# Performance work log

Measured on AMD Instinct MI355X. Metric: run time of the kernel, lower is better.

## Reference

```python
import jax, jax.numpy as jnp
import numpy as np

EPS = 1e-5

def _conv2d(x, w, b, pad):
    # NCHW conv, stride 1
    out = jax.lax.conv_general_dilated(x, w, (1, 1), [(pad, pad), (pad, pad)],
                                       dimension_numbers=('NCHW', 'OIHW', 'NCHW'))
    return out + b[None, :, None, None]

def _deform_conv2d(x, offset, mask, weight, bias, pad):
    # torchvision.ops.deform_conv2d (modulated, stride=1, dilation=1)
    B, C, H, W = x.shape
    O, _, K, _ = weight.shape
    kk = K * K
    off = offset.reshape(B, kk, 2, H, W)
    dy, dx = off[:, :, 0], off[:, :, 1]          # [B,kk,H,W]
    ki = (jnp.arange(kk) // K).astype(x.dtype)
    kj = (jnp.arange(kk) % K).astype(x.dtype)
    hh = jnp.arange(H, dtype=x.dtype)
    ww = jnp.arange(W, dtype=x.dtype)
    ys = dy + (hh[None, :, None] + ki[:, None, None] - pad)[None]  # [B,kk,H,W]
    xs = dx + (ww[None, None, :] + kj[:, None, None] - pad)[None]
    y0 = jnp.floor(ys); x0 = jnp.floor(xs)
    wy = ys - y0; wx = xs - x0
    xf = x.reshape(B, C, H * W)

    def gather(yi, xi):
        valid = ((yi >= 0) & (yi <= H - 1) & (xi >= 0) & (xi <= W - 1)).astype(x.dtype)
        yc = jnp.clip(yi, 0, H - 1).astype(jnp.int32)
        xc = jnp.clip(xi, 0, W - 1).astype(jnp.int32)
        idx = (yc * W + xc).reshape(B, -1)
        v = jax.vmap(lambda f, i: f[:, i])(xf, idx).reshape(B, C, kk, H, W)
        return v * valid[:, None]

    one = jnp.asarray(1.0, x.dtype)
    sampled = (gather(y0, x0) * ((one - wy) * (one - wx))[:, None]
               + gather(y0, x0 + 1) * ((one - wy) * wx)[:, None]
               + gather(y0 + 1, x0) * (wy * (one - wx))[:, None]
               + gather(y0 + 1, x0 + 1) * (wy * wx)[:, None])
    sampled = sampled * mask[:, None]            # modulation
    out = jnp.einsum('bckhw,ock->bohw', sampled, weight.reshape(O, C, kk))
    return out + bias[None, :, None, None]

def setup_inputs() -> dict:
    key = jax.random.key(0)
    ks = jax.random.split(key, 7)
    B, C, H, W = 8, 768, 32, 32
    x = jax.random.normal(ks[0], (B, C, H, W), jnp.float32)
    proj_w = jax.random.normal(ks[1], (768, 768, 3, 3), jnp.float32) * 0.02
    proj_b = jax.random.normal(ks[2], (768,), jnp.float32) * 0.02
    offset_w = jax.random.normal(ks[3], (18, 768, 3, 3), jnp.float32) * 0.01
    offset_b = jax.random.normal(ks[4], (18,), jnp.float32) * 0.01
    mask_w = jax.random.normal(ks[5], (9, 768, 3, 3), jnp.float32) * 0.01
    mask_b = jax.random.normal(ks[6], (9,), jnp.float32) * 0.01
    gamma = jnp.ones((768,), jnp.float32)
    beta = jnp.zeros((768,), jnp.float32)
    return {"x": x, "proj_w": proj_w, "proj_b": proj_b, "offset_w": offset_w,
            "offset_b": offset_b, "mask_w": mask_w, "mask_b": mask_b,
            "gamma": gamma, "beta": beta}

def reference(x, proj_w, proj_b, offset_w, offset_b, mask_w, mask_b, gamma, beta):
    pad = 1
    H, W = x.shape[-2], x.shape[-1]
    max_off = float(min(H, W) // 4)
    offset = jnp.clip(_conv2d(x, offset_w, offset_b, pad), -max_off, max_off)
    mask = 2.0 * jax.nn.sigmoid(_conv2d(x, mask_w, mask_b, pad))
    y = _deform_conv2d(x, offset, mask, proj_w, proj_b, pad)
    # SyncBatchNorm (training-mode batch statistics, biased var)
    mean = jnp.mean(y, axis=(0, 2, 3))
    var = jnp.var(y, axis=(0, 2, 3))
    yn = (y - mean[None, :, None, None]) * jax.lax.rsqrt(var + EPS)[None, :, None, None]
    yn = yn * gamma[None, :, None, None] + beta[None, :, None, None]
    return x + jax.nn.gelu(yn, approximate=False)
```

## Files before the change

kernel.cpp:

```cpp
#include <hip/hip_runtime.h>
#include <math.h>

typedef __attribute__((ext_vector_type(4))) float f32x4;
typedef __attribute__((ext_vector_type(8))) short s16x8;
typedef __attribute__((ext_vector_type(4))) unsigned int u32x4;
typedef unsigned short ushort_t;

#define HW   1024
#define C_IN 768
#define B_N  8

__device__ inline ushort_t f2bf(float f) {
    unsigned u = __builtin_bit_cast(unsigned, f);
    unsigned r = u + 0x7FFFu + ((u >> 16) & 1u);
    return (ushort_t)(r >> 16);
}
__device__ inline float bf2f(short s) {
    return __builtin_bit_cast(float, ((unsigned)(ushort_t)s) << 16);
}

__global__ __launch_bounds__(256) void prepack_xt(
    const float* __restrict__ x, ushort_t* __restrict__ xt)
{
    __shared__ ushort_t tile[64][66];
    int bid = blockIdx.x;
    int b  = bid / 192;
    int r  = bid % 192;
    int cg = r / 16, pg = r % 16;
    int c0 = cg * 64, p0 = pg * 64;
    int t = threadIdx.x;
#pragma unroll
    for (int i = 0; i < 16; ++i) {
        int idx = t + i * 256;
        int cr = idx >> 6, col = idx & 63;
        tile[cr][col] = f2bf(x[(((size_t)b * C_IN + c0 + cr) << 10) + p0 + col]);
    }
    __syncthreads();
#pragma unroll
    for (int i = 0; i < 16; ++i) {
        int idx = t + i * 256;
        int pr = idx >> 6, col = idx & 63;
        xt[((size_t)(b << 10) + p0 + pr) * C_IN + c0 + col] = tile[col][pr];
    }
}

__global__ __launch_bounds__(256) void prepack_proj(
    const float* __restrict__ pw, ushort_t* __restrict__ A)
{
    int t = blockIdx.x * 256 + threadIdx.x;
    int lane = t & 63;
    int smi  = t >> 6;
    int s  = smi / 48, mf = smi - s * 48;
    int o  = mf * 16 + (lane & 15);
    int k0 = s * 32 + ((lane >> 4) << 3);
    int tap = k0 / 768;
    int c   = k0 - tap * 768;
    const float* src = pw + (size_t)o * 6912 + (size_t)c * 9 + tap;
    s16x8 pk;
#pragma unroll
    for (int e = 0; e < 8; ++e) pk[e] = (short)f2bf(src[e * 9]);
    *(s16x8*)(A + (size_t)smi * 512 + lane * 8) = pk;
}

__global__ __launch_bounds__(256) void prepack_om(
    const float* __restrict__ offw, const float* __restrict__ mskw,
    ushort_t* __restrict__ A2)
{
    int t = blockIdx.x * 256 + threadIdx.x;
    int lane = t & 63;
    int smi  = t >> 6;
    int s  = smi >> 1, mf = smi & 1;
    int oc = mf * 16 + (lane & 15);
    int k0 = s * 32 + ((lane >> 4) << 3);
    int tap = k0 / 768;
    int c   = k0 - tap * 768;
    s16x8 pk;
#pragma unroll
    for (int e = 0; e < 8; ++e) pk[e] = 0;
    if (oc < 27) {
        const float* src = (oc < 18)
            ? offw + ((size_t)oc        * 768 + c) * 9 + tap
            : mskw + ((size_t)(oc - 18) * 768 + c) * 9 + tap;
#pragma unroll
        for (int e = 0; e < 8; ++e) pk[e] = (short)f2bf(src[e * 9]);
    }
    *(s16x8*)(A2 + (size_t)smi * 512 + lane * 8) = pk;
}

__global__ __launch_bounds__(256) void offmask_mfma(
    const ushort_t* __restrict__ xt, const ushort_t* __restrict__ A2,
    const float* __restrict__ offb, const float* __restrict__ mbias,
    float* __restrict__ offs, float* __restrict__ maskb)
{
    int bid = blockIdx.x;
    int b = bid >> 5, pt = bid & 31;
    int p0 = pt << 5;
    int t = threadIdx.x, lane = t & 63, wv = t >> 6;
    int mf = wv >> 1, nf = wv & 1;
    int q = lane >> 4;
    int px = p0 + nf * 16 + (lane & 15);
    int h = px >> 5, w = px & 31;
    const char* xb = (const char*)xt + (size_t)b * (HW * 1536);
    f32x4 acc = (f32x4){0.f, 0.f, 0.f, 0.f};

    for (int tap = 0; tap < 9; ++tap) {
        int yy = h + tap / 3 - 1, xx = w + tap % 3 - 1;
        bool ok = (yy >= 0 && yy < 32 && xx >= 0 && xx < 32);
        int pos = ok ? (yy * 32 + xx) : 0;
        const char* bp = xb + (size_t)pos * 1536 + q * 16;
        for (int cs = 0; cs < 24; ++cs) {
            int s = tap * 24 + cs;
            s16x8 bf;
            if (ok) bf = *(const s16x8*)(bp + cs * 64);
            else    bf = (s16x8){0, 0, 0, 0, 0, 0, 0, 0};
            s16x8 af = *(const s16x8*)(A2 + ((size_t)(s * 2 + mf) * 64 + lane) * 8);
            acc = __builtin_amdgcn_mfma_f32_16x16x32_bf16(af, bf, acc, 0, 0, 0);
        }
    }
#pragma unroll
    for (int r = 0; r < 4; ++r) {
        int oc = mf * 16 + ((lane >> 4) << 2) + r;
        if (oc < 18) {
            float v = acc[r] + offb[oc];
            v = fminf(fmaxf(v, -8.f), 8.f);
            offs[((b * 18 + oc) << 10) + px] = v;
        } else if (oc < 27) {
            float v = acc[r] + mbias[oc - 18];
            maskb[((b * 9 + oc - 18) << 10) + px] = 2.f / (1.f + expf(-v));
        }
    }
}

__global__ __launch_bounds__(512, 4) void deform_mfma(
    const ushort_t* __restrict__ xt, const ushort_t* __restrict__ Amat,
    const float* __restrict__ offs, const float* __restrict__ maskb,
    float* __restrict__ y)
{
    __shared__ float4 meta_w[576];
    __shared__ int4   meta_i[576];
    __shared__ __align__(16) ushort_t Bs[2][64][64];

    int id = blockIdx.x;
    int b = id & 7;
    int pxt = (id >> 3) & 15;
    int otile = id >> 7;
    int p0 = pxt << 6;
    int t = threadIdx.x, lane = t & 63, wv = t >> 6;
    int wm = wv >> 1, wn = wv & 1;
    int q4 = lane >> 4;

    int bpx = wv * 8 + (lane >> 3);
    int oct = lane & 7;
    const int wchunk = (oct ^ (bpx & 7)) * 8;

    for (int i = t; i < 576; i += 512) {
        int k = i >> 6, j = i & 63;
        int hw = p0 + j, h = hw >> 5, w = hw & 31;
        float dy = offs[((b * 18 + 2 * k) << 10) + hw];
        float dx = offs[((b * 18 + 2 * k + 1) << 10) + hw];
        float m  = maskb[((b * 9 + k) << 10) + hw];
        float ys = dy + (float)(h + k / 3 - 1);
        float xs = dx + (float)(w + k % 3 - 1);
        float fy = floorf(ys), fx = floorf(xs);
        float wy = ys - fy, wx = xs - fx;
        int iy0 = (int)fy, ix0 = (int)fx;
        int iy1 = iy0 + 1, ix1 = ix0 + 1;
        float vy0 = (iy0 >= 0 && iy0 < 32) ? 1.f : 0.f;
        float vy1 = (iy1 >= 0 && iy1 < 32) ? 1.f : 0.f;
        float vx0 = (ix0 >= 0 && ix0 < 32) ? 1.f : 0.f;
        float vx1 = (ix1 >= 0 && ix1 < 32) ? 1.f : 0.f;
        int cy0 = min(max(iy0, 0), 31), cx0 = min(max(ix0, 0), 31);
        int cy1 = min(max(iy1, 0), 31), cx1 = min(max(ix1, 0), 31);
        float4 wv4;
        wv4.x = (1.f - wy) * (1.f - wx) * m * vy0 * vx0;
        wv4.y = (1.f - wy) * wx         * m * vy0 * vx1;
        wv4.z = wy         * (1.f - wx) * m * vy1 * vx0;
        wv4.w = wy         * wx         * m * vy1 * vx1;
        meta_w[i] = wv4;
        meta_i[i] = make_int4((cy0 * 32 + cx0) * 1536, (cy0 * 32 + cx1) * 1536,
                              (cy1 * 32 + cx0) * 1536, (cy1 * 32 + cx1) * 1536);
    }
    asm volatile("s_waitcnt lgkmcnt(0)" ::: "memory");
    __builtin_amdgcn_s_barrier();

    f32x4 acc[3][2];
#pragma unroll
    for (int f = 0; f < 3; ++f)
#pragma unroll
        for (int n = 0; n < 2; ++n) acc[f][n] = (f32x4){0.f, 0.f, 0.f, 0.f};

    const char* xb = (const char*)xt + (size_t)b * (HW * 1536);
    const int afrag0 = otile * 12 + wm * 3;

    s16x8 ga0, ga1, ga2, ga3, gb0, gb1, gb2, gb3;
    float4 w4a, w4b;

#define WBAR() do { asm volatile("s_waitcnt lgkmcnt(0)" ::: "memory"); \
                    __builtin_amdgcn_s_barrier(); } while (0)

#define ISSUE(G0, G1, G2, G3, W4, qq) do {                                  \
    int nt_ = (qq) / 12, nc_ = (qq) - nt_ * 12;                             \
    W4 = meta_w[nt_ * 64 + bpx];                                            \
    int4 i4_ = meta_i[nt_ * 64 + bpx];                                      \
    const char* bsrc_ = xb + nc_ * 128 + oct * 16;                          \
    G0 = *(const s16x8*)(bsrc_ + i4_.x);                                    \
    G1 = *(const s16x8*)(bsrc_ + i4_.y);                                    \
    G2 = *(const s16x8*)(bsrc_ + i4_.z);                                    \
    G3 = *(const s16x8*)(bsrc_ + i4_.w);                                    \
} while (0)

#define BUILD(G0, G1, G2, G3, W4, BUF) do {                                 \
    u32x4 bw_;                                                              \
    _Pragma("unroll")                                                       \
    for (int e2 = 0; e2 < 4; ++e2) {                                        \
        float v0_ = W4.x * bf2f(G0[2*e2])   + W4.y * bf2f(G1[2*e2])         \
                  + W4.z * bf2f(G2[2*e2])   + W4.w * bf2f(G3[2*e2]);        \
        float v1_ = W4.x * bf2f(G0[2*e2+1]) + W4.y * bf2f(G1[2*e2+1])       \
                  + W4.z * bf2f(G2[2*e2+1]) + W4.w * bf2f(G3[2*e2+1]);      \
        unsigned rr_;                                                       \
        asm("v_cvt_pk_bf16_f32 %0, %1, %2" : "=v"(rr_) : "v"(v0_), "v"(v1_)); \
        bw_[e2] = rr_;                                                      \
    }                                                                       \
    *(u32x4*)&Bs[BUF][bpx][wchunk] = bw_;                                   \
} while (0)

#define MFMA_PHASE(P, BUF) do {                                             \
    _Pragma("unroll")                                                       \
    for (int kk = 0; kk < 2; ++kk) {                                        \
        int s_ = 2 * (P) + kk;                                              \
        const s16x8* ap_ = (const s16x8*)(Amat +                            \
            ((size_t)(s_ * 48 + afrag0) * 64 + lane) * 8);                  \
        s16x8 a0_ = ap_[0], a1_ = ap_[64], a2_ = ap_[128];                  \
        int rc_ = ((kk * 4 + q4) ^ (lane & 7)) * 8;                         \
        s16x8 b0_ = *(const s16x8*)&Bs[BUF][wn * 32 + (lane & 15)][rc_];    \
        s16x8 b1_ = *(const s16x8*)&Bs[BUF][wn * 32 + 16 + (lane & 15)][rc_]; \
        acc[0][0] = __builtin_amdgcn_mfma_f32_16x16x32_bf16(a0_, b0_, acc[0][0], 0, 0, 0); \
        acc[0][1] = __builtin_amdgcn_mfma_f32_16x16x32_bf16(a0_, b1_, acc[0][1], 0, 0, 0); \
        acc[1][0] = __builtin_amdgcn_mfma_f32_16x16x32_bf16(a1_, b0_, acc[1][0], 0, 0, 0); \
        acc[1][1] = __builtin_amdgcn_mfma_f32_16x16x32_bf16(a1_, b1_, acc[1][1], 0, 0, 0); \
        acc[2][0] = __builtin_amdgcn_mfma_f32_16x16x32_bf16(a2_, b0_, acc[2][0], 0, 0, 0); \
        acc[2][1] = __builtin_amdgcn_mfma_f32_16x16x32_bf16(a2_, b1_, acc[2][1], 0, 0, 0); \
    }                                                                       \
} while (0)

    ISSUE(ga0, ga1, ga2, ga3, w4a, 0);
    ISSUE(gb0, gb1, gb2, gb3, w4b, 1);
    BUILD(ga0, ga1, ga2, ga3, w4a, 0);
    WBAR();

    for (int pp = 0; pp < 54; ++pp) {
        int pe = 2 * pp;
        if (pp < 53) ISSUE(ga0, ga1, ga2, ga3, w4a, pe + 2);
        MFMA_PHASE(pe, 0);
        BUILD(gb0, gb1, gb2, gb3, w4b, 1);
        WBAR();

        int po = pe + 1;
        if (pp < 53) ISSUE(gb0, gb1, gb2, gb3, w4b, po + 2);
        MFMA_PHASE(po, 1);
        if (pp < 53) BUILD(ga0, ga1, ga2, ga3, w4a, 0);
        WBAR();
    }

    int pxo = p0 + wn * 32 + (lane & 15);
    int obase = otile * 192 + wm * 48;
#pragma unroll
    for (int f = 0; f < 3; ++f) {
        int orow = obase + f * 16 + ((lane >> 4) << 2);
#pragma unroll
        for (int r = 0; r < 4; ++r) {
            size_t rowoff = ((size_t)(b * 768 + orow + r) << 10);
            y[rowoff + pxo]      = acc[f][0][r];
            y[rowoff + pxo + 16] = acc[f][1][r];
        }
    }
#undef WBAR
#undef ISSUE
#undef BUILD
#undef MFMA_PHASE
}

__global__ __launch_bounds__(256) void stats_kernel(
    const float* __restrict__ y, float* __restrict__ stats)
{
    int o = blockIdx.x;
    int tid = threadIdx.x;
    float s1 = 0.f, s2 = 0.f;
    for (int i = tid; i < B_N * HW; i += 256) {
        int b = i >> 10, hw = i & 1023;
        float v = y[(((size_t)b * 768 + o) << 10) + hw];
        s1 += v; s2 += v * v;
    }
#pragma unroll
    for (int off = 32; off > 0; off >>= 1) {
        s1 += __shfl_down(s1, off);
        s2 += __shfl_down(s2, off);
    }
    __shared__ float ls1[4], ls2[4];
    int wid = tid >> 6, lane = tid & 63;
    if (lane == 0) { ls1[wid] = s1; ls2[wid] = s2; }
    __syncthreads();
    if (tid == 0) {
        float t1 = ls1[0] + ls1[1] + ls1[2] + ls1[3];
        float t2 = ls2[0] + ls2[1] + ls2[2] + ls2[3];
        float mean = t1 * (1.0f / 8192.0f);
        float var  = t2 * (1.0f / 8192.0f) - mean * mean;
        stats[o]       = mean;
        stats[768 + o] = 1.0f / sqrtf(var + 1e-5f);
    }
}

__global__ __launch_bounds__(256) void finalize_kernel(
    const float* __restrict__ x, const float* __restrict__ stats,
    const float* __restrict__ gamma, const float* __restrict__ beta,
    float* __restrict__ y)
{
    const int total4 = B_N * 768 * HW / 4;
    for (int f = blockIdx.x * 256 + threadIdx.x; f < total4;
         f += gridDim.x * 256) {
        int e = f << 2;
        int o = (e >> 10) % 768;
        float mean = stats[o], rstd = stats[768 + o];
        float ga = gamma[o], be = beta[o];
        float4 v  = ((const float4*)y)[f];
        float4 xv = ((const float4*)x)[f];
        float4 r;
        {
            float yn = (v.x - mean) * rstd * ga + be;
            r.x = xv.x + 0.5f * yn * (1.0f + erff(yn * 0.70710678f));
        }
        {
            float yn = (v.y - mean) * rstd * ga + be;
            r.y = xv.y + 0.5f * yn * (1.0f + erff(yn * 0.70710678f));
        }
        {
            float yn = (v.z - mean) * rstd * ga + be;
            r.z = xv.z + 0.5f * yn * (1.0f + erff(yn * 0.70710678f));
        }
        {
            float yn = (v.w - mean) * rstd * ga + be;
            r.w = xv.w + 0.5f * yn * (1.0f + erff(yn * 0.70710678f));
        }
        ((float4*)y)[f] = r;
    }
}

extern "C" void kernel_launch(void* const* d_in, const int* in_sizes, int n_in,
                              void* d_out, int out_size, void* d_ws, size_t ws_size,
                              hipStream_t stream)
{
    const float* x        = (const float*)d_in[0];
    const float* proj_w   = (const float*)d_in[1];
    const float* offset_w = (const float*)d_in[3];
    const float* offset_b = (const float*)d_in[4];
    const float* mask_w   = (const float*)d_in[5];
    const float* mask_b   = (const float*)d_in[6];
    const float* gamma    = (const float*)d_in[7];
    const float* beta     = (const float*)d_in[8];

    char* ws = (char*)d_ws;
    float*    offs  = (float*)(ws);
    float*    maskb = (float*)(ws + 589824);
    float*    stats = (float*)(ws + 884736);
    ushort_t* A     = (ushort_t*)(ws + 890880);
    ushort_t* A2    = (ushort_t*)(ws + 11507712);
    ushort_t* xt    = (ushort_t*)(ws + 11950080);
    float* y = (float*)d_out;

    prepack_xt<<<1536, 256, 0, stream>>>(x, xt);
    prepack_om<<<108, 256, 0, stream>>>(offset_w, mask_w, A2);
    prepack_proj<<<2592, 256, 0, stream>>>(proj_w, A);
    offmask_mfma<<<256, 256, 0, stream>>>(xt, A2, offset_b, mask_b, offs, maskb);
    deform_mfma<<<512, 512, 0, stream>>>(xt, A, offs, maskb, y);
    stats_kernel<<<768, 256, 0, stream>>>(y, stats);
    finalize_kernel<<<2048, 256, 0, stream>>>(x, stats, gamma, beta, y);
}
```

Measured before the change: 270.6 us.

## Share each bilinear-sampled B tile across 384 output channels with 1024-thread blocks

The deformable-conv MFMA kernel now launches 256 blocks of 1024 threads instead of 512 blocks of 512, so each block covers 384 output channels instead of 192. Each sampled B tile is built once and consumed by 16 waves, which halves the redundant bilinear gather and interpolation work across output-channel tiles. Each thread now gathers and interpolates 4 bf16 values instead of 8. MFMA phases are also wrapped in s_setprio to favour matrix issue over the gather waves. The trade-off is fewer, larger blocks and potentially more barrier contention among 16 waves per block.

```diff
diff --git a/kernel.cpp b/kernel.cpp
--- a/kernel.cpp
+++ b/kernel.cpp
@@ -3,7 +3,7 @@
 
 typedef __attribute__((ext_vector_type(4))) float f32x4;
 typedef __attribute__((ext_vector_type(8))) short s16x8;
-typedef __attribute__((ext_vector_type(4))) unsigned int u32x4;
+typedef __attribute__((ext_vector_type(4))) short s16x4;
 typedef unsigned short ushort_t;
 
 #define HW   1024
@@ -131,7 +131,7 @@
     }
 }
 
-__global__ __launch_bounds__(512, 4) void deform_mfma(
+__global__ __launch_bounds__(1024, 4) void deform_mfma(
     const ushort_t* __restrict__ xt, const ushort_t* __restrict__ Amat,
     const float* __restrict__ offs, const float* __restrict__ maskb,
     float* __restrict__ y)
@@ -145,15 +145,16 @@
     int pxt = (id >> 3) & 15;
     int otile = id >> 7;
     int p0 = pxt << 6;
-    int t = threadIdx.x, lane = t & 63, wv = t >> 6;
-    int wm = wv >> 1, wn = wv & 1;
+    int t = threadIdx.x, lane = t & 63, wvid = t >> 6;
+    int wm = wvid >> 1, wn = wvid & 1;
     int q4 = lane >> 4;
 
-    int bpx = wv * 8 + (lane >> 3);
-    int oct = lane & 7;
-    const int wchunk = (oct ^ (bpx & 7)) * 8;
-
-    for (int i = t; i < 576; i += 512) {
+    int bpx  = t >> 4;
+    int sub  = t & 15;
+    int oct  = sub >> 1, half = sub & 1;
+    const int wchunk = (oct ^ (bpx & 7)) * 8 + half * 4;
+
+    for (int i = t; i < 576; i += 1024) {
         int k = i >> 6, j = i & 63;
         int hw = p0 + j, h = hw >> 5, w = hw & 31;
         float dy = offs[((b * 18 + 2 * k) << 10) + hw];
@@ -190,9 +191,9 @@
         for (int n = 0; n < 2; ++n) acc[f][n] = (f32x4){0.f, 0.f, 0.f, 0.f};
 
     const char* xb = (const char*)xt + (size_t)b * (HW * 1536);
-    const int afrag0 = otile * 12 + wm * 3;
-
-    s16x8 ga0, ga1, ga2, ga3, gb0, gb1, gb2, gb3;
+    const int afrag0 = otile * 24 + wm * 3;
+
+    s16x4 ga0, ga1, ga2, ga3, gb0, gb1, gb2, gb3;
     float4 w4a, w4b;
 
 #define WBAR() do { asm volatile("s_waitcnt lgkmcnt(0)" ::: "memory"); \
@@ -202,29 +203,36 @@
     int nt_ = (qq) / 12, nc_ = (qq) - nt_ * 12;                             \
     W4 = meta_w[nt_ * 64 + bpx];                                            \
     int4 i4_ = meta_i[nt_ * 64 + bpx];                                      \
-    const char* bsrc_ = xb + nc_ * 128 + oct * 16;                          \
-    G0 = *(const s16x8*)(bsrc_ + i4_.x);                                    \
-    G1 = *(const s16x8*)(bsrc_ + i4_.y);                                    \
-    G2 = *(const s16x8*)(bsrc_ + i4_.z);                                    \
-    G3 = *(const s16x8*)(bsrc_ + i4_.w);                                    \
+    const char* bsrc_ = xb + nc_ * 128 + sub * 8;                           \
+    G0 = *(const s16x4*)(bsrc_ + i4_.x);                                    \
+    G1 = *(const s16x4*)(bsrc_ + i4_.y);                                    \
+    G2 = *(const s16x4*)(bsrc_ + i4_.z);                                    \
+    G3 = *(const s16x4*)(bsrc_ + i4_.w);                                    \
 } while (0)
 
 #define BUILD(G0, G1, G2, G3, W4, BUF) do {                                 \
-    u32x4 bw_;                                                              \
-    _Pragma("unroll")                                                       \
-    for (int e2 = 0; e2 < 4; ++e2) {                                        \
-        float v0_ = W4.x * bf2f(G0[2*e2])   + W4.y * bf2f(G1[2*e2])         \
-                  + W4.z * bf2f(G2[2*e2])   + W4.w * bf2f(G3[2*e2]);        \
-        float v1_ = W4.x * bf2f(G0[2*e2+1]) + W4.y * bf2f(G1[2*e2+1])       \
-                  + W4.z * bf2f(G2[2*e2+1]) + W4.w * bf2f(G3[2*e2+1]);      \
-        unsigned rr_;                                                       \
-        asm("v_cvt_pk_bf16_f32 %0, %1, %2" : "=v"(rr_) : "v"(v0_), "v"(v1_)); \
-        bw_[e2] = rr_;                                                      \
+    uint2 bw_;                                                              \
+    unsigned r0_, r1_;                                                      \
+    {                                                                       \
+        float v0_ = W4.x * bf2f(G0[0]) + W4.y * bf2f(G1[0])                 \
+                  + W4.z * bf2f(G2[0]) + W4.w * bf2f(G3[0]);                \
+        float v1_ = W4.x * bf2f(G0[1]) + W4.y * bf2f(G1[1])                 \
+                  + W4.z * bf2f(G2[1]) + W4.w * bf2f(G3[1]);                \
+        asm("v_cvt_pk_bf16_f32 %0, %1, %2" : "=v"(r0_) : "v"(v0_), "v"(v1_)); \
     }                                                                       \
-    *(u32x4*)&Bs[BUF][bpx][wchunk] = bw_;                                   \
+    {                                                                       \
+        float v0_ = W4.x * bf2f(G0[2]) + W4.y * bf2f(G1[2])                 \
+                  + W4.z * bf2f(G2[2]) + W4.w * bf2f(G3[2]);                \
+        float v1_ = W4.x * bf2f(G0[3]) + W4.y * bf2f(G1[3])                 \
+                  + W4.z * bf2f(G2[3]) + W4.w * bf2f(G3[3]);                \
+        asm("v_cvt_pk_bf16_f32 %0, %1, %2" : "=v"(r1_) : "v"(v0_), "v"(v1_)); \
+    }                                                                       \
+    bw_.x = r0_; bw_.y = r1_;                                               \
+    *(uint2*)&Bs[BUF][bpx][wchunk] = bw_;                                   \
 } while (0)
 
 #define MFMA_PHASE(P, BUF) do {                                             \
+    __builtin_amdgcn_s_setprio(1);                                          \
     _Pragma("unroll")                                                       \
     for (int kk = 0; kk < 2; ++kk) {                                        \
         int s_ = 2 * (P) + kk;                                              \
@@ -241,6 +249,7 @@
         acc[2][0] = __builtin_amdgcn_mfma_f32_16x16x32_bf16(a2_, b0_, acc[2][0], 0, 0, 0); \
         acc[2][1] = __builtin_amdgcn_mfma_f32_16x16x32_bf16(a2_, b1_, acc[2][1], 0, 0, 0); \
     }                                                                       \
+    __builtin_amdgcn_s_setprio(0);                                          \
 } while (0)
 
     ISSUE(ga0, ga1, ga2, ga3, w4a, 0);
@@ -263,7 +272,7 @@
     }
 
     int pxo = p0 + wn * 32 + (lane & 15);
-    int obase = otile * 192 + wm * 48;
+    int obase = otile * 384 + wm * 48;
 #pragma unroll
     for (int f = 0; f < 3; ++f) {
         int orow = obase + f * 16 + ((lane >> 4) << 2);
@@ -371,7 +380,7 @@
     prepack_om<<<108, 256, 0, stream>>>(offset_w, mask_w, A2);
     prepack_proj<<<2592, 256, 0, stream>>>(proj_w, A);
     offmask_mfma<<<256, 256, 0, stream>>>(xt, A2, offset_b, mask_b, offs, maskb);
-    deform_mfma<<<512, 512, 0, stream>>>(xt, A, offs, maskb, y);
+    deform_mfma<<<256, 1024, 0, stream>>>(xt, A, offs, maskb, y);
     stats_kernel<<<768, 256, 0, stream>>>(y, stats);
     finalize_kernel<<<2048, 256, 0, stream>>>(x, stats, gamma, beta, y);
 }
```

New measurement: 306.3 us. 13.2% more time.

## Double output-channel tile in deform GEMM and stage proj weight prepack through LDS

Applied to the files above, without the earlier changes.

The deform_mfma kernel now computes 384 output channels per block instead of 192. Each block builds the bilinear-sampled B tile once and reuses it across twice as many MFMA fragments, which halves the redundant gathers and interpolation and halves the grid. Separately, prepack_proj loads contiguous rows of proj_w into shared memory and then transposes them, replacing strided global reads. The cost is more accumulator registers per thread and fewer blocks in flight, which may reduce occupancy and latency hiding.

```diff
diff --git a/kernel.cpp b/kernel.cpp
--- a/kernel.cpp
+++ b/kernel.cpp
@@ -47,19 +47,32 @@
 __global__ __launch_bounds__(256) void prepack_proj(
     const float* __restrict__ pw, ushort_t* __restrict__ A)
 {
-    int t = blockIdx.x * 256 + threadIdx.x;
-    int lane = t & 63;
-    int smi  = t >> 6;
-    int s  = smi / 48, mf = smi - s * 48;
-    int o  = mf * 16 + (lane & 15);
-    int k0 = s * 32 + ((lane >> 4) << 3);
-    int tap = k0 / 768;
-    int c   = k0 - tap * 768;
-    const float* src = pw + (size_t)o * 6912 + (size_t)c * 9 + tap;
-    s16x8 pk;
-#pragma unroll
-    for (int e = 0; e < 8; ++e) pk[e] = (short)f2bf(src[e * 9]);
-    *(s16x8*)(A + (size_t)smi * 512 + lane * 8) = pk;
+    __shared__ ushort_t tile[16][584];
+    int bid = blockIdx.x;
+    int mf = bid / 12, cblk = bid - mf * 12;
+    int t = threadIdx.x;
+    const float* src = pw + (size_t)mf * 16 * 6912 + cblk * 576;
+#pragma unroll
+    for (int i = 0; i < 36; ++i) {
+        int f = i * 256 + t;
+        int orow = f / 576, col = f - orow * 576;
+        tile[orow][col] = f2bf(src[(size_t)orow * 6912 + col]);
+    }
+    __syncthreads();
+    int lane = t & 63, fi0 = t >> 6;
+    for (int it = 0; it < 5; ++it) {
+        int fidx = it * 4 + fi0;
+        if (fidx < 18) {
+            int tap = fidx >> 1, half = fidx & 1;
+            int s = tap * 24 + cblk * 2 + half;
+            int cl0 = half * 32 + ((lane >> 4) << 3);
+            s16x8 pk;
+#pragma unroll
+            for (int e = 0; e < 8; ++e)
+                pk[e] = (short)tile[lane & 15][(cl0 + e) * 9 + tap];
+            *(s16x8*)(A + ((size_t)(s * 48 + mf) * 64 + lane) * 8) = pk;
+        }
+    }
 }
 
 __global__ __launch_bounds__(256) void prepack_om(
@@ -183,14 +196,14 @@
     asm volatile("s_waitcnt lgkmcnt(0)" ::: "memory");
     __builtin_amdgcn_s_barrier();
 
-    f32x4 acc[3][2];
-#pragma unroll
-    for (int f = 0; f < 3; ++f)
+    f32x4 acc[6][2];
+#pragma unroll
+    for (int f = 0; f < 6; ++f)
 #pragma unroll
         for (int n = 0; n < 2; ++n) acc[f][n] = (f32x4){0.f, 0.f, 0.f, 0.f};
 
     const char* xb = (const char*)xt + (size_t)b * (HW * 1536);
-    const int afrag0 = otile * 12 + wm * 3;
+    const int afrag0 = otile * 24 + wm * 6;
 
     s16x8 ga0, ga1, ga2, ga3, gb0, gb1, gb2, gb3;
     float4 w4a, w4b;
@@ -230,7 +243,8 @@
         int s_ = 2 * (P) + kk;                                              \
         const s16x8* ap_ = (const s16x8*)(Amat +                            \
             ((size_t)(s_ * 48 + afrag0) * 64 + lane) * 8);                  \
-        s16x8 a0_ = ap_[0], a1_ = ap_[64], a2_ = ap_[128];                  \
+        s16x8 a0_ = ap_[0],   a1_ = ap_[64],  a2_ = ap_[128];               \
+        s16x8 a3_ = ap_[192], a4_ = ap_[256], a5_ = ap_[320];               \
         int rc_ = ((kk * 4 + q4) ^ (lane & 7)) * 8;                         \
         s16x8 b0_ = *(const s16x8*)&Bs[BUF][wn * 32 + (lane & 15)][rc_];    \
         s16x8 b1_ = *(const s16x8*)&Bs[BUF][wn * 32 + 16 + (lane & 15)][rc_]; \
@@ -240,6 +254,12 @@
         acc[1][1] = __builtin_amdgcn_mfma_f32_16x16x32_bf16(a1_, b1_, acc[1][1], 0, 0, 0); \
         acc[2][0] = __builtin_amdgcn_mfma_f32_16x16x32_bf16(a2_, b0_, acc[2][0], 0, 0, 0); \
         acc[2][1] = __builtin_amdgcn_mfma_f32_16x16x32_bf16(a2_, b1_, acc[2][1], 0, 0, 0); \
+        acc[3][0] = __builtin_amdgcn_mfma_f32_16x16x32_bf16(a3_, b0_, acc[3][0], 0, 0, 0); \
+        acc[3][1] = __builtin_amdgcn_mfma_f32_16x16x32_bf16(a3_, b1_, acc[3][1], 0, 0, 0); \
+        acc[4][0] = __builtin_amdgcn_mfma_f32_16x16x32_bf16(a4_, b0_, acc[4][0], 0, 0, 0); \
+        acc[4][1] = __builtin_amdgcn_mfma_f32_16x16x32_bf16(a4_, b1_, acc[4][1], 0, 0, 0); \
+        acc[5][0] = __builtin_amdgcn_mfma_f32_16x16x32_bf16(a5_, b0_, acc[5][0], 0, 0, 0); \
+        acc[5][1] = __builtin_amdgcn_mfma_f32_16x16x32_bf16(a5_, b1_, acc[5][1], 0, 0, 0); \
     }                                                                       \
 } while (0)
 
@@ -263,9 +283,9 @@
     }
 
     int pxo = p0 + wn * 32 + (lane & 15);
-    int obase = otile * 192 + wm * 48;
-#pragma unroll
-    for (int f = 0; f < 3; ++f) {
+    int obase = otile * 384 + wm * 96;
+#pragma unroll
+    for (int f = 0; f < 6; ++f) {
         int orow = obase + f * 16 + ((lane >> 4) << 2);
 #pragma unroll
         for (int r = 0; r < 4; ++r) {
@@ -369,9 +389,9 @@
 
     prepack_xt<<<1536, 256, 0, stream>>>(x, xt);
     prepack_om<<<108, 256, 0, stream>>>(offset_w, mask_w, A2);
-    prepack_proj<<<2592, 256, 0, stream>>>(proj_w, A);
+    prepack_proj<<<576, 256, 0, stream>>>(proj_w, A);
     offmask_mfma<<<256, 256, 0, stream>>>(xt, A2, offset_b, mask_b, offs, maskb);
-    deform_mfma<<<512, 512, 0, stream>>>(xt, A, offs, maskb, y);
+    deform_mfma<<<256, 512, 0, stream>>>(xt, A, offs, maskb, y);
     stats_kernel<<<768, 256, 0, stream>>>(y, stats);
     finalize_kernel<<<2048, 256, 0, stream>>>(x, stats, gamma, beta, y);
 }
```

Result: slower. 305.2 us (+12.8%).
